# Kernel optimization log

Measured on AMD Instinct MI355X. Metric: run time of the kernel, lower is better.

## Reference

```python
import jax, jax.numpy as jnp
import numpy as np

N_LEVELS = 8
N_FEATS = 8            # features per level
BASE_RES = 16
PER_LEVEL_SCALE = 1.2599210739135742
LOG2_HASHMAP = 19
TABLE_PAD = 8192       # padded per-level table rows (>= max level size 6568)
N_POINTS = 262144


def _level_params(l):
    # tcnn: scale = base * s^l - 1 ; res = ceil(scale)+1 ; size = min(2^19, round_up(res^2, 8))
    scale = BASE_RES * (PER_LEVEL_SCALE ** l) - 1.0
    res = int(np.ceil(scale)) + 1
    size = min(1 << LOG2_HASHMAP, ((res * res + 7) // 8) * 8)
    return float(scale), res, size


def hashgrid_encode(x, table):
    """x: [N,2] in [0,1), table: [L, TABLE_PAD, F]. Returns [N, L*F]."""
    outs = []
    for l in range(N_LEVELS):
        scale, res, size = _level_params(l)
        pos = x * jnp.float32(scale) + jnp.float32(0.5)
        pg = jnp.floor(pos)
        frac = pos - pg
        pg = pg.astype(jnp.int32)
        # Smoothstep interpolation weights: t^2 (3 - 2t)
        w = frac * frac * (3.0 - 2.0 * frac)          # [N,2]
        feat = jnp.zeros((x.shape[0], N_FEATS), dtype=table.dtype)
        for dx in (0, 1):
            wx = w[:, 0] if dx else 1.0 - w[:, 0]
            for dy in (0, 1):
                wy = w[:, 1] if dy else 1.0 - w[:, 1]
                # dense grid index (all levels here fit the hashmap), modulo level size as in tcnn
                idx = ((pg[:, 0] + dx) + (pg[:, 1] + dy) * res) % size
                feat = feat + (wx * wy)[:, None] * table[l, idx]  # irregular gather
        outs.append(feat)
    return jnp.concatenate(outs, axis=-1)  # [N, 64]


def mlp(enc, W0, W1, W2, W3):
    h = jax.nn.relu(enc @ W0)
    h = jax.nn.relu(h @ W1)
    h = jax.nn.relu(h @ W2)
    return h @ W3  # linear output activation


def setup_inputs() -> dict:
    key = jax.random.key(0)
    ks = jax.random.split(key, 6)
    x = jax.random.uniform(ks[0], (N_POINTS, 2), dtype=jnp.float32)
    # tcnn initializes grid params ~ uniform(-1e-4, 1e-4); small values
    table = jax.random.normal(ks[1], (N_LEVELS, TABLE_PAD, N_FEATS), dtype=jnp.float32) * 1e-2
    W0 = jax.random.normal(ks[2], (64, 256), dtype=jnp.float32) * (1.0 / np.sqrt(64))
    W1 = jax.random.normal(ks[3], (256, 256), dtype=jnp.float32) * (1.0 / np.sqrt(256))
    W2 = jax.random.normal(ks[4], (256, 256), dtype=jnp.float32) * (1.0 / np.sqrt(256))
    W3 = jax.random.normal(ks[5], (256, 1), dtype=jnp.float32) * (1.0 / np.sqrt(256))
    return {"x": x, "table": table, "W0": W0, "W1": W1, "W2": W2, "W3": W3}


def reference(x, table, W0, W1, W2, W3):
    enc = hashgrid_encode(x, table)
    return mlp(enc, W0, W1, W2, W3)  # [N, 1]
```

## Files before the change

### kernel.cpp

```cpp
#include <hip/hip_runtime.h>
#include <cmath>


#define N_LEVELS 8
#define TABLE_PAD 8192
#define TILE_M 64
#define ACT_STRIDE 264

typedef __attribute__((ext_vector_type(8))) short short8;
typedef __attribute__((ext_vector_type(16))) float float16v;

#define LGKM0() asm volatile("s_waitcnt lgkmcnt(0)" ::: "memory")
#define CFENCE() asm volatile("" ::: "memory")

struct LevelParams {
  float scale[N_LEVELS];
  int   res[N_LEVELS];
  int   size[N_LEVELS];
};

__device__ __forceinline__ unsigned short f2bf(float f) {
  unsigned int u = __float_as_uint(f);
  u += 0x7fffu + ((u >> 16) & 1u);
  return (unsigned short)(u >> 16);
}
__device__ __forceinline__ unsigned int pack2bf(float a, float b) {
  a = a > 0.f ? a : 0.f;
  b = b > 0.f ? b : 0.f;
  return (unsigned int)f2bf(a) | ((unsigned int)f2bf(b) << 16);
}

__global__ void pack_weights_kernel(const float* __restrict__ W0,
                                    const float* __restrict__ W1,
                                    const float* __restrict__ W2,
                                    unsigned short* __restrict__ Wp) {
  int tid = blockIdx.x * blockDim.x + threadIdx.x;
  const float* src;
  int base, e;
  if (tid < 16384)        { src = W0; base = 0;     e = tid;         }
  else if (tid < 81920)   { src = W1; base = 16384; e = tid - 16384; }
  else if (tid < 147456)  { src = W2; base = 81920; e = tid - 81920; }
  else return;
  int ki = e & 15;
  int n  = (e >> 4) & 255;
  int kb = e >> 12;
  unsigned int u = __float_as_uint(src[(kb * 16 + ki) * 256 + n]);
  u += 0x7fffu + ((u >> 16) & 1u);
  Wp[base + e] = (unsigned short)(u >> 16);
}

__global__ __launch_bounds__(512, 6) void neural_field_kernel(
    const float* __restrict__ x,
    const float* __restrict__ table,
    const unsigned short* __restrict__ Wp,
    const float* __restrict__ W3,
    float* __restrict__ out,
    LevelParams P) {
  __shared__ unsigned short bufA[TILE_M * ACT_STRIDE];
  __shared__ float fsum[TILE_M * 9];

  const int t  = threadIdx.x;
  const int g0 = blockIdx.x * TILE_M;

  const int lane  = t & 63;
  const int w     = t >> 6;
  const int l31   = lane & 31;
  const int h8    = lane >> 5;
  const int wbase = w * 32;

  const int woff = (wbase + l31) * 16 + h8 * 8;

  {
    int p = t & 63;
    int l = t >> 6;
    float2 xy = ((const float2*)x)[g0 + p];
    float scale = P.scale[l];
    int res = P.res[l], size = P.size[l];
    float posx = xy.x * scale + 0.5f;
    float posy = xy.y * scale + 0.5f;
    float pgx = floorf(posx), pgy = floorf(posy);
    float fx = posx - pgx, fy = posy - pgy;
    float wx = fx * fx * (3.0f - 2.0f * fx);
    float wy = fy * fy * (3.0f - 2.0f * fy);
    int px = (int)pgx, py = (int)pgy;
    float acc[8] = {0, 0, 0, 0, 0, 0, 0, 0};
    for (int dy = 0; dy < 2; ++dy) {
      float wyv = dy ? wy : 1.0f - wy;
      for (int dx = 0; dx < 2; ++dx) {
        float wgt = (dx ? wx : 1.0f - wx) * wyv;
        int idx = (px + dx) + (py + dy) * res;
        if (idx >= size) idx -= size;
        const float4* tp =
            (const float4*)(table + ((size_t)l * TABLE_PAD + idx) * 8);
        float4 t0 = tp[0], t1 = tp[1];
        acc[0] += wgt * t0.x; acc[1] += wgt * t0.y;
        acc[2] += wgt * t0.z; acc[3] += wgt * t0.w;
        acc[4] += wgt * t1.x; acc[5] += wgt * t1.y;
        acc[6] += wgt * t1.z; acc[7] += wgt * t1.w;
      }
    }
    union { unsigned short s[8]; short8 v; } u;
    for (int j = 0; j < 8; ++j) u.s[j] = f2bf(acc[j]);
    *(short8*)&bufA[p * ACT_STRIDE + l * 8] = u.v;
  }

  LGKM0();
  __builtin_amdgcn_s_barrier();
  CFENCE();

  auto run_layer = [&](const unsigned short* Wpl, int KB,
                       bool inplace, bool fuse_final) {
    float16v acc[2];
#pragma unroll
    for (int j = 0; j < 16; ++j) { acc[0][j] = 0.f; acc[1][j] = 0.f; }

    const unsigned short* ap0 = &bufA[l31 * ACT_STRIDE + h8 * 8];
    const unsigned short* ap1 = ap0 + 32 * ACT_STRIDE;
    const unsigned short* wp  = Wpl + woff;

    short8 wr[5];
    wr[0] = *(const short8*)(wp);
    wr[1] = *(const short8*)(wp + 1 * 4096);
    wr[2] = (KB > 2) ? *(const short8*)(wp + 2 * 4096) : wr[0];
    wr[3] = (KB > 3) ? *(const short8*)(wp + 3 * 4096) : wr[0];
    short8 a0 = *(const short8*)(ap0);
    short8 a1 = *(const short8*)(ap1);

#pragma unroll
    for (int kb = 0; kb < KB; ++kb) {
      if (kb + 4 < KB)
        wr[(kb + 4) % 5] = *(const short8*)(wp + (kb + 4) * 4096);
      short8 b0, b1;
      if (kb + 1 < KB) {
        b0 = *(const short8*)(ap0 + (kb + 1) * 16);
        b1 = *(const short8*)(ap1 + (kb + 1) * 16);
      }
      const short8 wf = wr[kb % 5];
      acc[0] = __builtin_amdgcn_mfma_f32_32x32x16_bf16(wf, a0, acc[0],
                                                       0, 0, 0);
      acc[1] = __builtin_amdgcn_mfma_f32_32x32x16_bf16(wf, a1, acc[1],
                                                       0, 0, 0);
      if (kb + 1 < KB) { a0 = b0; a1 = b1; }
    }

    if (inplace) {
      __builtin_amdgcn_s_barrier();
      CFENCE();
    }

    if (!fuse_final) {
#pragma unroll
      for (int pt = 0; pt < 2; ++pt) {
        int m = pt * 32 + l31;
#pragma unroll
        for (int q = 0; q < 4; ++q) {
          int n0 = wbase + 8 * q + 4 * h8;
          uint2 pk;
          pk.x = pack2bf(acc[pt][4 * q + 0], acc[pt][4 * q + 1]);
          pk.y = pack2bf(acc[pt][4 * q + 2], acc[pt][4 * q + 3]);
          *(uint2*)&bufA[m * ACT_STRIDE + n0] = pk;
        }
      }
    } else {
      float part0 = 0.f, part1 = 0.f;
#pragma unroll
      for (int q = 0; q < 4; ++q) {
        float4 wv = *(const float4*)(W3 + wbase + 8 * q + 4 * h8);
        float w3v[4] = {wv.x, wv.y, wv.z, wv.w};
#pragma unroll
        for (int r = 0; r < 4; ++r) {
          float v0 = acc[0][4 * q + r]; v0 = v0 > 0.f ? v0 : 0.f;
          float v1 = acc[1][4 * q + r]; v1 = v1 > 0.f ? v1 : 0.f;
          part0 += v0 * w3v[r];
          part1 += v1 * w3v[r];
        }
      }
      part0 += __shfl_xor(part0, 32);
      part1 += __shfl_xor(part1, 32);
      float val = h8 ? part1 : part0;
      fsum[lane * 9 + w] = val;
    }
  };

  run_layer(Wp, 4, true, false);
  LGKM0();
  __builtin_amdgcn_s_barrier();
  CFENCE();
  run_layer(Wp + 16384, 16, true, false);
  LGKM0();
  __builtin_amdgcn_s_barrier();
  CFENCE();
  run_layer(Wp + 81920, 16, false, true);
  LGKM0();
  __builtin_amdgcn_s_barrier();
  CFENCE();

  {
    int p = t >> 3;
    int q = t & 7;
    float v = fsum[p * 9 + q];
    v += __shfl_xor(v, 1);
    v += __shfl_xor(v, 2);
    v += __shfl_xor(v, 4);
    if (q == 0) out[g0 + p] = v;
  }
}

extern "C" void kernel_launch(void* const* d_in, const int* in_sizes, int n_in,
                              void* d_out, int out_size, void* d_ws,
                              size_t ws_size, hipStream_t stream) {
  const float* x     = (const float*)d_in[0];
  const float* table = (const float*)d_in[1];
  const float* W0    = (const float*)d_in[2];
  const float* W1    = (const float*)d_in[3];
  const float* W2    = (const float*)d_in[4];
  const float* W3    = (const float*)d_in[5];
  float* out = (float*)d_out;
  int N = in_sizes[0] / 2;

  unsigned short* Wp = (unsigned short*)d_ws;

  LevelParams P;
  const double c = 1.2599210739135742;
  double m = 1.0;
  for (int l = 0; l < N_LEVELS; ++l) {
    double scale_d = 16.0 * m - 1.0;
    int res = (int)std::ceil(scale_d) + 1;
    long long sz = ((long long)res * res + 7) / 8 * 8;
    if (sz > (1LL << 19)) sz = 1LL << 19;
    P.scale[l] = (float)scale_d;
    P.res[l]   = res;
    P.size[l]  = (int)sz;
    m *= c;
  }

  hipLaunchKernelGGL(pack_weights_kernel, dim3(576), dim3(256), 0, stream,
                     W0, W1, W2, Wp);
  hipLaunchKernelGGL(neural_field_kernel, dim3(N / TILE_M), dim3(512), 0,
                     stream, x, table, Wp, W3, out, P);
}
```

Baseline: 166.7 us.

## Make kernel persistent with all MLP weights held in registers across tiles

Converts the kernel into a persistent grid of 256 blocks that loop over point tiles. All bf16 weight fragments for the three hidden layers and the W3 vector are loaded into registers once per block, so they are not re-read from global memory for every tile. This uses about 144 extra VGPRs per thread (36 short8 values), and the launch bound is lowered to 2 blocks per SM. The cost is lower occupancy and less latency hiding for the irregular hash-table gathers.

```diff
diff --git a/kernel.cpp b/kernel.cpp
--- a/kernel.cpp
+++ b/kernel.cpp
@@ -49,18 +49,17 @@
   Wp[base + e] = (unsigned short)(u >> 16);
 }
 
-__global__ __launch_bounds__(512, 6) void neural_field_kernel(
+__global__ __launch_bounds__(512, 2) void neural_field_kernel(
     const float* __restrict__ x,
     const float* __restrict__ table,
     const unsigned short* __restrict__ Wp,
     const float* __restrict__ W3,
     float* __restrict__ out,
-    LevelParams P) {
+    LevelParams P, int nTiles) {
   __shared__ unsigned short bufA[TILE_M * ACT_STRIDE];
   __shared__ float fsum[TILE_M * 9];
 
-  const int t  = threadIdx.x;
-  const int g0 = blockIdx.x * TILE_M;
+  const int t = threadIdx.x;
 
   const int lane  = t & 63;
   const int w     = t >> 6;
@@ -70,45 +69,25 @@
 
   const int woff = (wbase + l31) * 16 + h8 * 8;
 
-  {
-    int p = t & 63;
-    int l = t >> 6;
-    float2 xy = ((const float2*)x)[g0 + p];
-    float scale = P.scale[l];
-    int res = P.res[l], size = P.size[l];
-    float posx = xy.x * scale + 0.5f;
-    float posy = xy.y * scale + 0.5f;
-    float pgx = floorf(posx), pgy = floorf(posy);
-    float fx = posx - pgx, fy = posy - pgy;
-    float wx = fx * fx * (3.0f - 2.0f * fx);
-    float wy = fy * fy * (3.0f - 2.0f * fy);
-    int px = (int)pgx, py = (int)pgy;
-    float acc[8] = {0, 0, 0, 0, 0, 0, 0, 0};
-    for (int dy = 0; dy < 2; ++dy) {
-      float wyv = dy ? wy : 1.0f - wy;
-      for (int dx = 0; dx < 2; ++dx) {
-        float wgt = (dx ? wx : 1.0f - wx) * wyv;
-        int idx = (px + dx) + (py + dy) * res;
-        if (idx >= size) idx -= size;
-        const float4* tp =
-            (const float4*)(table + ((size_t)l * TABLE_PAD + idx) * 8);
-        float4 t0 = tp[0], t1 = tp[1];
-        acc[0] += wgt * t0.x; acc[1] += wgt * t0.y;
-        acc[2] += wgt * t0.z; acc[3] += wgt * t0.w;
-        acc[4] += wgt * t1.x; acc[5] += wgt * t1.y;
-        acc[6] += wgt * t1.z; acc[7] += wgt * t1.w;
-      }
-    }
-    union { unsigned short s[8]; short8 v; } u;
-    for (int j = 0; j < 8; ++j) u.s[j] = f2bf(acc[j]);
-    *(short8*)&bufA[p * ACT_STRIDE + l * 8] = u.v;
+  short8 wr0[4], wr1[16], wr2[16];
+#pragma unroll
+  for (int i = 0; i < 4; ++i)
+    wr0[i] = *(const short8*)(Wp + woff + i * 4096);
+#pragma unroll
+  for (int i = 0; i < 16; ++i)
+    wr1[i] = *(const short8*)(Wp + 16384 + woff + i * 4096);
+#pragma unroll
+  for (int i = 0; i < 16; ++i)
+    wr2[i] = *(const short8*)(Wp + 81920 + woff + i * 4096);
+  float w3f[16];
+#pragma unroll
+  for (int q = 0; q < 4; ++q) {
+    float4 wv = *(const float4*)(W3 + wbase + 8 * q + 4 * h8);
+    w3f[4 * q + 0] = wv.x; w3f[4 * q + 1] = wv.y;
+    w3f[4 * q + 2] = wv.z; w3f[4 * q + 3] = wv.w;
   }
 
-  LGKM0();
-  __builtin_amdgcn_s_barrier();
-  CFENCE();
-
-  auto run_layer = [&](const unsigned short* Wpl, int KB,
+  auto run_layer = [&](const short8* wfr, int KB,
                        bool inplace, bool fuse_final) {
     float16v acc[2];
 #pragma unroll
@@ -116,29 +95,20 @@
 
     const unsigned short* ap0 = &bufA[l31 * ACT_STRIDE + h8 * 8];
     const unsigned short* ap1 = ap0 + 32 * ACT_STRIDE;
-    const unsigned short* wp  = Wpl + woff;
-
-    short8 wr[5];
-    wr[0] = *(const short8*)(wp);
-    wr[1] = *(const short8*)(wp + 1 * 4096);
-    wr[2] = (KB > 2) ? *(const short8*)(wp + 2 * 4096) : wr[0];
-    wr[3] = (KB > 3) ? *(const short8*)(wp + 3 * 4096) : wr[0];
+
     short8 a0 = *(const short8*)(ap0);
     short8 a1 = *(const short8*)(ap1);
 
 #pragma unroll
     for (int kb = 0; kb < KB; ++kb) {
-      if (kb + 4 < KB)
-        wr[(kb + 4) % 5] = *(const short8*)(wp + (kb + 4) * 4096);
       short8 b0, b1;
       if (kb + 1 < KB) {
         b0 = *(const short8*)(ap0 + (kb + 1) * 16);
         b1 = *(const short8*)(ap1 + (kb + 1) * 16);
       }
-      const short8 wf = wr[kb % 5];
-      acc[0] = __builtin_amdgcn_mfma_f32_32x32x16_bf16(wf, a0, acc[0],
+      acc[0] = __builtin_amdgcn_mfma_f32_32x32x16_bf16(wfr[kb], a0, acc[0],
                                                        0, 0, 0);
-      acc[1] = __builtin_amdgcn_mfma_f32_32x32x16_bf16(wf, a1, acc[1],
+      acc[1] = __builtin_amdgcn_mfma_f32_32x32x16_bf16(wfr[kb], a1, acc[1],
                                                        0, 0, 0);
       if (kb + 1 < KB) { a0 = b0; a1 = b1; }
     }
@@ -164,16 +134,11 @@
     } else {
       float part0 = 0.f, part1 = 0.f;
 #pragma unroll
-      for (int q = 0; q < 4; ++q) {
-        float4 wv = *(const float4*)(W3 + wbase + 8 * q + 4 * h8);
-        float w3v[4] = {wv.x, wv.y, wv.z, wv.w};
-#pragma unroll
-        for (int r = 0; r < 4; ++r) {
-          float v0 = acc[0][4 * q + r]; v0 = v0 > 0.f ? v0 : 0.f;
-          float v1 = acc[1][4 * q + r]; v1 = v1 > 0.f ? v1 : 0.f;
-          part0 += v0 * w3v[r];
-          part1 += v1 * w3v[r];
-        }
+      for (int j = 0; j < 16; ++j) {
+        float v0 = acc[0][j]; v0 = v0 > 0.f ? v0 : 0.f;
+        float v1 = acc[1][j]; v1 = v1 > 0.f ? v1 : 0.f;
+        part0 += v0 * w3f[j];
+        part1 += v1 * w3f[j];
       }
       part0 += __shfl_xor(part0, 32);
       part1 += __shfl_xor(part1, 32);
@@ -182,27 +147,69 @@
     }
   };
 
-  run_layer(Wp, 4, true, false);
-  LGKM0();
-  __builtin_amdgcn_s_barrier();
-  CFENCE();
-  run_layer(Wp + 16384, 16, true, false);
-  LGKM0();
-  __builtin_amdgcn_s_barrier();
-  CFENCE();
-  run_layer(Wp + 81920, 16, false, true);
-  LGKM0();
-  __builtin_amdgcn_s_barrier();
-  CFENCE();
-
-  {
-    int p = t >> 3;
-    int q = t & 7;
-    float v = fsum[p * 9 + q];
-    v += __shfl_xor(v, 1);
-    v += __shfl_xor(v, 2);
-    v += __shfl_xor(v, 4);
-    if (q == 0) out[g0 + p] = v;
+  for (int tile = blockIdx.x; tile < nTiles; tile += gridDim.x) {
+    const int g0 = tile * TILE_M;
+
+    {
+      int p = t & 63;
+      int l = t >> 6;
+      float2 xy = ((const float2*)x)[g0 + p];
+      float scale = P.scale[l];
+      int res = P.res[l], size = P.size[l];
+      float posx = xy.x * scale + 0.5f;
+      float posy = xy.y * scale + 0.5f;
+      float pgx = floorf(posx), pgy = floorf(posy);
+      float fx = posx - pgx, fy = posy - pgy;
+      float wx = fx * fx * (3.0f - 2.0f * fx);
+      float wy = fy * fy * (3.0f - 2.0f * fy);
+      int px = (int)pgx, py = (int)pgy;
+      float acc[8] = {0, 0, 0, 0, 0, 0, 0, 0};
+      for (int dy = 0; dy < 2; ++dy) {
+        float wyv = dy ? wy : 1.0f - wy;
+        for (int dx = 0; dx < 2; ++dx) {
+          float wgt = (dx ? wx : 1.0f - wx) * wyv;
+          int idx = (px + dx) + (py + dy) * res;
+          if (idx >= size) idx -= size;
+          const float4* tp =
+              (const float4*)(table + ((size_t)l * TABLE_PAD + idx) * 8);
+          float4 t0 = tp[0], t1 = tp[1];
+          acc[0] += wgt * t0.x; acc[1] += wgt * t0.y;
+          acc[2] += wgt * t0.z; acc[3] += wgt * t0.w;
+          acc[4] += wgt * t1.x; acc[5] += wgt * t1.y;
+          acc[6] += wgt * t1.z; acc[7] += wgt * t1.w;
+        }
+      }
+      union { unsigned short s[8]; short8 v; } u;
+      for (int j = 0; j < 8; ++j) u.s[j] = f2bf(acc[j]);
+      *(short8*)&bufA[p * ACT_STRIDE + l * 8] = u.v;
+    }
+
+    LGKM0();
+    __builtin_amdgcn_s_barrier();
+    CFENCE();
+
+    run_layer(wr0, 4, true, false);
+    LGKM0();
+    __builtin_amdgcn_s_barrier();
+    CFENCE();
+    run_layer(wr1, 16, true, false);
+    LGKM0();
+    __builtin_amdgcn_s_barrier();
+    CFENCE();
+    run_layer(wr2, 16, false, true);
+    LGKM0();
+    __builtin_amdgcn_s_barrier();
+    CFENCE();
+
+    {
+      int p = t >> 3;
+      int q = t & 7;
+      float v = fsum[p * 9 + q];
+      v += __shfl_xor(v, 1);
+      v += __shfl_xor(v, 2);
+      v += __shfl_xor(v, 4);
+      if (q == 0) out[g0 + p] = v;
+    }
   }
 }
 
@@ -236,6 +243,6 @@
 
   hipLaunchKernelGGL(pack_weights_kernel, dim3(576), dim3(256), 0, stream,
                      W0, W1, W2, Wp);
-  hipLaunchKernelGGL(neural_field_kernel, dim3(N / TILE_M), dim3(512), 0,
-                     stream, x, table, Wp, W3, out, P);
-}
+  hipLaunchKernelGGL(neural_field_kernel, dim3(256), dim3(512), 0,
+                     stream, x, table, Wp, W3, out, P, N / TILE_M);
+}
```

Result: no change. 165.5 us (-0.7%).
